# Optimization experiments

Hardware: AMD Instinct MI355X
Metric: run time of the kernel (lower is better)

The kernel has to match this reference:

```python
import jax, jax.numpy as jnp
import numpy as np

D_MODEL = 1024
N_HEAD = 16
B, T = 1, 4096


def setup_inputs() -> dict:
    key = jax.random.key(0)
    ks = jax.random.split(key, 12)
    s = 1.0 / np.sqrt(D_MODEL)
    inp = {
        "q": jax.random.normal(ks[0], (B, T, D_MODEL), jnp.float32),
        "k": jax.random.normal(ks[1], (B, T, D_MODEL), jnp.float32),
        "v": jax.random.normal(ks[2], (B, T, D_MODEL), jnp.float32),
        # causal mask: True = keep, False = mask out (mask==0 path in torch)
        "mask": jnp.tril(jnp.ones((T, T), dtype=bool))[None, None],
        "w_q": jax.random.uniform(ks[3], (D_MODEL, D_MODEL), jnp.float32, -s, s),
        "b_q": jax.random.uniform(ks[4], (D_MODEL,), jnp.float32, -s, s),
        "w_k": jax.random.uniform(ks[5], (D_MODEL, D_MODEL), jnp.float32, -s, s),
        "b_k": jax.random.uniform(ks[6], (D_MODEL,), jnp.float32, -s, s),
        "w_v": jax.random.uniform(ks[7], (D_MODEL, D_MODEL), jnp.float32, -s, s),
        "b_v": jax.random.uniform(ks[8], (D_MODEL,), jnp.float32, -s, s),
        "w_o": jax.random.uniform(ks[9], (D_MODEL, D_MODEL), jnp.float32, -s, s),
        "b_o": jax.random.uniform(ks[10], (D_MODEL,), jnp.float32, -s, s),
    }
    return inp


def reference(q, k, v, mask, w_q, b_q, w_k, b_k, w_v, b_v, w_o, b_o):
    batch, time, d_model = q.shape
    n_d = d_model // N_HEAD
    # Linear projections (torch Linear: x @ W.T + b)
    qh = (q @ w_q.T + b_q).reshape(batch, time, N_HEAD, n_d).transpose(0, 2, 1, 3)
    kh = (k @ w_k.T + b_k).reshape(batch, -1, N_HEAD, n_d).transpose(0, 2, 1, 3)
    vh = (v @ w_v.T + b_v).reshape(batch, -1, N_HEAD, n_d).transpose(0, 2, 1, 3)
    # [B, H, Tq, Tk] score matrix (naive, materialized as in original)
    score = jnp.einsum("bhqd,bhkd->bhqk", qh, kh) / jnp.sqrt(jnp.float32(n_d))
    score = jnp.where(mask, score, jnp.float32(-10000.0))
    attn = jax.nn.softmax(score, axis=-1)
    out = jnp.einsum("bhqk,bhkd->bhqd", attn, vh)
    out = out.transpose(0, 2, 1, 3).reshape(batch, time, d_model)
    return out @ w_o.T + b_o
```

## Files before the change

kernel.cpp:

```cpp
#include <hip/hip_runtime.h>

typedef unsigned short u16;
typedef unsigned int u32;
typedef __bf16 b16x8 __attribute__((ext_vector_type(8)));
typedef float f32x4 __attribute__((ext_vector_type(4)));
typedef u32 u32x4 __attribute__((ext_vector_type(4)));

__device__ __forceinline__ u16 f2b(float f) {
    u32 u = __builtin_bit_cast(u32, f);
    u32 r = (u + 0x7fffu + ((u >> 16) & 1u)) >> 16;
    return (u16)r;
}
__device__ __forceinline__ b16x8 frag(u32x4 x) { return __builtin_bit_cast(b16x8, x); }

__device__ __forceinline__ void gld16(const u16* g, u16* l) {
    __builtin_amdgcn_global_load_lds((const __attribute__((address_space(1))) u32*)g,
                                     (__attribute__((address_space(3))) u32*)l, 16, 0, 0);
}

#define SEQ 4096
#define DMODEL 1024
#define NHEAD 16
#define HDIM 64
#define QK_SCALE 0.18033688011112042f

__global__ void cvt3(const float* __restrict__ s0, const float* __restrict__ s1,
                     const float* __restrict__ s2, u16* __restrict__ d0,
                     u16* __restrict__ d1, u16* __restrict__ d2, int n4) {
    const int t = blockIdx.y;
    const float* s = (t == 0) ? s0 : (t == 1) ? s1 : s2;
    u16* d = (t == 0) ? d0 : (t == 1) ? d1 : d2;
    const int stride = gridDim.x * blockDim.x;
    for (int i = blockIdx.x * blockDim.x + threadIdx.x; i < n4; i += stride) {
        float4 f = ((const float4*)s)[i];
        ushort4 o;
        o.x = f2b(f.x); o.y = f2b(f.y); o.z = f2b(f.z); o.w = f2b(f.w);
        ((ushort4*)d)[i] = o;
    }
}

__global__ void cvt4(const float* __restrict__ s0, const float* __restrict__ s1,
                     const float* __restrict__ s2, const float* __restrict__ s3,
                     u16* __restrict__ d0, u16* __restrict__ d1,
                     u16* __restrict__ d2, u16* __restrict__ d3, int n4) {
    const int t = blockIdx.y;
    const float* s = (t == 0) ? s0 : (t == 1) ? s1 : (t == 2) ? s2 : s3;
    u16* d = (t == 0) ? d0 : (t == 1) ? d1 : (t == 2) ? d2 : d3;
    const int stride = gridDim.x * blockDim.x;
    for (int i = blockIdx.x * blockDim.x + threadIdx.x; i < n4; i += stride) {
        float4 f = ((const float4*)s)[i];
        ushort4 o;
        o.x = f2b(f.x); o.y = f2b(f.y); o.z = f2b(f.z); o.w = f2b(f.w);
        ((ushort4*)d)[i] = o;
    }
}

template <int NN, bool BIAS_ROW, int OUT>
__global__ __launch_bounds__(256) void gemm_bt(const u16* __restrict__ A,
                                               const u16* __restrict__ Bt,
                                               const float* __restrict__ bias,
                                               void* __restrict__ Cv, float scale) {
    constexpr int K = 1024;
    __shared__ __attribute__((aligned(16))) u16 As[128 * 32];
    __shared__ __attribute__((aligned(16))) u16 Bs[128 * 32];

    const int tid = threadIdx.x;
    const int wave = tid >> 6, lane = tid & 63;
    const int quad = lane >> 4, l16 = lane & 15;
    const int wr = wave >> 1, wc = wave & 1;
    const int m0 = blockIdx.y * 128, n0 = blockIdx.x * 128;

    f32x4 acc[4][4] = {};

    const int srow = tid >> 2;
    const int scol = (tid & 3) * 8;
    const u16* Aptr = A + (size_t)(m0 + srow) * K + scol;
    const u16* Bptr = Bt + (size_t)(n0 + srow) * K + scol;
    u16* AsW0 = &As[wave * 512];
    u16* AsW1 = &As[2048 + wave * 512];
    u16* BsW0 = &Bs[wave * 512];
    u16* BsW1 = &Bs[2048 + wave * 512];

    for (int k0 = 0; k0 < K; k0 += 32) {
        __syncthreads();
        gld16(Aptr + k0, AsW0);
        gld16(Aptr + k0 + (size_t)64 * K, AsW1);
        gld16(Bptr + k0, BsW0);
        gld16(Bptr + k0 + (size_t)64 * K, BsW1);
        __syncthreads();

        b16x8 af[4], bf[4];
#pragma unroll
        for (int mt = 0; mt < 4; ++mt)
            af[mt] = frag(*(const u32x4*)&As[(wr * 64 + mt * 16 + l16) * 32 + quad * 8]);
#pragma unroll
        for (int nt = 0; nt < 4; ++nt)
            bf[nt] = frag(*(const u32x4*)&Bs[(wc * 64 + nt * 16 + l16) * 32 + quad * 8]);
#pragma unroll
        for (int mt = 0; mt < 4; ++mt)
#pragma unroll
            for (int nt = 0; nt < 4; ++nt)
                acc[mt][nt] = __builtin_amdgcn_mfma_f32_16x16x32_bf16(af[mt], bf[nt], acc[mt][nt], 0, 0, 0);
    }

#pragma unroll
    for (int nt = 0; nt < 4; ++nt) {
        const int col = n0 + wc * 64 + nt * 16 + l16;
        const float bcol = BIAS_ROW ? 0.f : bias[col];
#pragma unroll
        for (int mt = 0; mt < 4; ++mt) {
            const int row0 = m0 + wr * 64 + mt * 16 + quad * 4;
#pragma unroll
            for (int r = 0; r < 4; ++r) {
                const float bv = BIAS_ROW ? bias[row0 + r] : bcol;
                float v = (acc[mt][nt][r] + bv) * scale;
                if (OUT == 2) {
                    ((float*)Cv)[(size_t)(row0 + r) * NN + col] = v;
                } else if (OUT == 1) {
                    ((u16*)Cv)[((size_t)(col >> 6) * SEQ + (row0 + r)) * HDIM + (col & 63)] = f2b(v);
                } else {
                    ((u16*)Cv)[(size_t)(row0 + r) * NN + col] = f2b(v);
                }
            }
        }
    }
}

__global__ __launch_bounds__(256) void flash_attn(const u16* __restrict__ Q,
                                                  const u16* __restrict__ K,
                                                  const u16* __restrict__ V,
                                                  u16* __restrict__ O) {
    constexpr int LDK = 72;
    __shared__ __attribute__((aligned(16))) u16 Ks[64 * LDK];
    __shared__ __attribute__((aligned(16))) u16 Vs[64 * LDK];
    __shared__ __attribute__((aligned(16))) u16 Ps[128 * LDK];

    const int tid = threadIdx.x;
    const int wave = tid >> 6, lane = tid & 63;
    const int quad = lane >> 4, l16 = lane & 15;

    const int idx = blockIdx.x;
    const int h = idx & (NHEAD - 1);
    const int qt = (SEQ / 128 - 1) - (idx >> 4);
    const int q0 = qt * 128;

    const u16* Qh = Q + (size_t)h * SEQ * HDIM;
    const u16* Kh = K + (size_t)h * SEQ * HDIM;
    const u16* Vh = V + (size_t)h * HDIM * SEQ;

    b16x8 qf[2][2];
#pragma unroll
    for (int mf = 0; mf < 2; ++mf) {
        const u16* qp = Qh + (size_t)(q0 + wave * 32 + mf * 16 + l16) * HDIM + quad * 8;
        qf[mf][0] = frag(*(const u32x4*)qp);
        qf[mf][1] = frag(*(const u32x4*)(qp + 32));
    }
    b16x8 onesf;
    {
        u32x4 o = {0x3F803F80u, 0x3F803F80u, 0x3F803F80u, 0x3F803F80u};
        onesf = frag(o);
    }

    f32x4 acc[2][4] = {};
    f32x4 accl[2] = {};

    const int r0 = tid >> 3;
    const int c0 = (tid & 7) * 8;

    const int nkt = 2 * qt + 2;
    for (int kt = 0; kt < nkt; ++kt) {
        const int k0 = kt * 64;
        u32x4 ka = *(const u32x4*)(Kh + (size_t)(k0 + r0) * HDIM + c0);
        u32x4 kb = *(const u32x4*)(Kh + (size_t)(k0 + r0 + 32) * HDIM + c0);
        u32x4 va = *(const u32x4*)(Vh + (size_t)r0 * SEQ + k0 + c0);
        u32x4 vb = *(const u32x4*)(Vh + (size_t)(r0 + 32) * SEQ + k0 + c0);
        __syncthreads();
        *(u32x4*)&Ks[r0 * LDK + c0] = ka;
        *(u32x4*)&Ks[(r0 + 32) * LDK + c0] = kb;
        *(u32x4*)&Vs[r0 * LDK + c0] = va;
        *(u32x4*)&Vs[(r0 + 32) * LDK + c0] = vb;
        __syncthreads();

        f32x4 s[2][4];
#pragma unroll
        for (int nt = 0; nt < 4; ++nt) {
            b16x8 kf0 = frag(*(const u32x4*)&Ks[(nt * 16 + l16) * LDK + quad * 8]);
            b16x8 kf1 = frag(*(const u32x4*)&Ks[(nt * 16 + l16) * LDK + 32 + quad * 8]);
#pragma unroll
            for (int mf = 0; mf < 2; ++mf) {
                f32x4 z = {};
                z = __builtin_amdgcn_mfma_f32_16x16x32_bf16(qf[mf][0], kf0, z, 0, 0, 0);
                z = __builtin_amdgcn_mfma_f32_16x16x32_bf16(qf[mf][1], kf1, z, 0, 0, 0);
                s[mf][nt] = z;
            }
        }

        if (kt >= 2 * qt) {
#pragma unroll
            for (int nt = 0; nt < 4; ++nt) {
                const int j = k0 + nt * 16 + l16;
#pragma unroll
                for (int mf = 0; mf < 2; ++mf) {
                    const int ib = q0 + wave * 32 + mf * 16 + quad * 4;
#pragma unroll
                    for (int r = 0; r < 4; ++r)
                        if (j > ib + r) s[mf][nt][r] = -1e30f;
                }
            }
        }

#pragma unroll
        for (int mf = 0; mf < 2; ++mf)
#pragma unroll
            for (int nt = 0; nt < 4; ++nt)
#pragma unroll
                for (int r = 0; r < 4; ++r) {
                    const float p = __builtin_amdgcn_exp2f(s[mf][nt][r] - 16.0f);
                    Ps[(wave * 32 + mf * 16 + quad * 4 + r) * LDK + nt * 16 + l16] = f2b(p);
                }
        __syncthreads();

#pragma unroll
        for (int ks = 0; ks < 2; ++ks) {
            b16x8 a[2];
#pragma unroll
            for (int mf = 0; mf < 2; ++mf) {
                a[mf] = frag(*(const u32x4*)&Ps[(wave * 32 + mf * 16 + l16) * LDK + ks * 32 + quad * 8]);
                accl[mf] = __builtin_amdgcn_mfma_f32_16x16x32_bf16(a[mf], onesf, accl[mf], 0, 0, 0);
            }
#pragma unroll
            for (int dt = 0; dt < 4; ++dt) {
                b16x8 b = frag(*(const u32x4*)&Vs[(dt * 16 + l16) * LDK + ks * 32 + quad * 8]);
#pragma unroll
                for (int mf = 0; mf < 2; ++mf)
                    acc[mf][dt] = __builtin_amdgcn_mfma_f32_16x16x32_bf16(a[mf], b, acc[mf][dt], 0, 0, 0);
            }
        }
    }

#pragma unroll
    for (int mf = 0; mf < 2; ++mf)
#pragma unroll
        for (int dt = 0; dt < 4; ++dt)
#pragma unroll
            for (int r = 0; r < 4; ++r) {
                const int row = q0 + wave * 32 + mf * 16 + quad * 4 + r;
                const int col = h * HDIM + dt * 16 + l16;
                O[(size_t)row * DMODEL + col] = f2b(acc[mf][dt][r] / accl[mf][r]);
            }
}

extern "C" void kernel_launch(void* const* d_in, const int* in_sizes, int n_in,
                              void* d_out, int out_size, void* d_ws, size_t ws_size,
                              hipStream_t stream) {
    const float* qkv[3] = {nullptr, nullptr, nullptr};
    const float* wts[4] = {nullptr, nullptr, nullptr, nullptr};
    const float* bss[4] = {nullptr, nullptr, nullptr, nullptr};
    int nqkv = 0, nw = 0, nb = 0;
    for (int i = 0; i < n_in; ++i) {
        const int sz = in_sizes[i];
        if (sz == SEQ * DMODEL) {
            if (nqkv < 3) qkv[nqkv++] = (const float*)d_in[i];
        } else if (sz == DMODEL * DMODEL) {
            if (nw < 4) wts[nw++] = (const float*)d_in[i];
        } else if (sz == DMODEL) {
            if (nb < 4) bss[nb++] = (const float*)d_in[i];
        }
    }

    u16* ws = (u16*)d_ws;
    const size_t ELEMS = (size_t)SEQ * DMODEL;
    const size_t WELEMS = (size_t)DMODEL * DMODEL;

    size_t off = 0;
    u16* cq = ws + off; off += ELEMS;
    u16* ck = ws + off; off += ELEMS;
    u16* cv = ws + off; off += ELEMS;
    u16* cwq = ws + off; off += WELEMS;
    u16* cwk = ws + off; off += WELEMS;
    u16* cwv = ws + off; off += WELEMS;
    u16* cwo = ws + off; off += WELEMS;
    u16* qh = ws + off; off += ELEMS;
    u16* kh = ws + off; off += ELEMS;
    u16* vt = ws + off; off += ELEMS;
    u16* att = ws + off; off += ELEMS;

    dim3 blk(256);
    cvt3<<<dim3(1024, 3), blk, 0, stream>>>(qkv[0], qkv[1], qkv[2], cq, ck, cv,
                                            (int)(ELEMS / 4));
    cvt4<<<dim3(256, 4), blk, 0, stream>>>(wts[0], wts[1], wts[2], wts[3],
                                           cwq, cwk, cwv, cwo, (int)(WELEMS / 4));

    dim3 gM(DMODEL / 128, SEQ / 128);
    dim3 gV(SEQ / 128, DMODEL / 128);
    gemm_bt<DMODEL, false, 1><<<gM, blk, 0, stream>>>(cq, cwq, bss[0], qh, QK_SCALE);
    gemm_bt<DMODEL, false, 1><<<gM, blk, 0, stream>>>(ck, cwk, bss[1], kh, 1.0f);
    gemm_bt<SEQ, true, 0><<<gV, blk, 0, stream>>>(cwv, cv, bss[2], vt, 1.0f);
    flash_attn<<<dim3(NHEAD * (SEQ / 128)), blk, 0, stream>>>(qh, kh, vt, att);
    gemm_bt<DMODEL, false, 2><<<gM, blk, 0, stream>>>(att, cwo, bss[3], d_out, 1.0f);
}
```

Before: 363.1 us.

## Split causal attention KV range across blocks, batch QKV GEMMs, narrow output GEMM

Flash attention now splits the causal key range of the later query tiles into up to four chunks, each handled by its own block. Each block writes unnormalized partial outputs and row sums, and a new combine kernel sums them and normalizes. The aim is to balance the triangular workload and give the GPU more blocks. The three QKV projection GEMMs are merged into one launch over a z dimension, and the output GEMM uses 128x64 tiles so it launches more blocks. The trade-off is an extra kernel plus partial-result traffic through workspace buffers, which reuse the converted input regions.

```diff
diff --git a/kernel.cpp b/kernel.cpp
--- a/kernel.cpp
+++ b/kernel.cpp
@@ -10,6 +10,10 @@
     u32 u = __builtin_bit_cast(u32, f);
     u32 r = (u + 0x7fffu + ((u >> 16) & 1u)) >> 16;
     return (u16)r;
+}
+__device__ __forceinline__ float b2f(u16 h) {
+    u32 u = ((u32)h) << 16;
+    return __builtin_bit_cast(float, u);
 }
 __device__ __forceinline__ b16x8 frag(u32x4 x) { return __builtin_bit_cast(b16x8, x); }
 
@@ -55,20 +59,34 @@
     }
 }
 
-template <int NN, bool BIAS_ROW, int OUT>
-__global__ __launch_bounds__(256) void gemm_bt(const u16* __restrict__ A,
-                                               const u16* __restrict__ Bt,
-                                               const float* __restrict__ bias,
-                                               void* __restrict__ Cv, float scale) {
+__global__ __launch_bounds__(256) void gemm_qkv(
+    const u16* __restrict__ cq, const u16* __restrict__ ck, const u16* __restrict__ cv,
+    const u16* __restrict__ cwq, const u16* __restrict__ cwk, const u16* __restrict__ cwv,
+    const float* __restrict__ bq, const float* __restrict__ bk, const float* __restrict__ bv,
+    u16* __restrict__ qh, u16* __restrict__ kh, u16* __restrict__ vt) {
     constexpr int K = 1024;
     __shared__ __attribute__((aligned(16))) u16 As[128 * 32];
     __shared__ __attribute__((aligned(16))) u16 Bs[128 * 32];
+
+    const int z = blockIdx.z;
+    const u16* A = (z == 0) ? cq : (z == 1) ? ck : cwv;
+    const u16* Bt = (z == 0) ? cwq : (z == 1) ? cwk : cv;
+    const float* bias = (z == 0) ? bq : (z == 1) ? bk : bv;
+
+    int m0, n0;
+    if (z < 2) {
+        m0 = blockIdx.y * 128;
+        n0 = blockIdx.x * 128;
+    } else {
+        const int id = blockIdx.y * 8 + blockIdx.x;
+        m0 = (id >> 5) * 128;
+        n0 = (id & 31) * 128;
+    }
 
     const int tid = threadIdx.x;
     const int wave = tid >> 6, lane = tid & 63;
     const int quad = lane >> 4, l16 = lane & 15;
     const int wr = wave >> 1, wc = wave & 1;
-    const int m0 = blockIdx.y * 128, n0 = blockIdx.x * 128;
 
     f32x4 acc[4][4] = {};
 
@@ -103,25 +121,86 @@
                 acc[mt][nt] = __builtin_amdgcn_mfma_f32_16x16x32_bf16(af[mt], bf[nt], acc[mt][nt], 0, 0, 0);
     }
 
+    u16* C = (z == 0) ? qh : kh;
+    const float sc = (z == 0) ? QK_SCALE : 1.0f;
 #pragma unroll
     for (int nt = 0; nt < 4; ++nt) {
         const int col = n0 + wc * 64 + nt * 16 + l16;
-        const float bcol = BIAS_ROW ? 0.f : bias[col];
+        const float bcol = (z < 2) ? bias[col] : 0.f;
 #pragma unroll
         for (int mt = 0; mt < 4; ++mt) {
             const int row0 = m0 + wr * 64 + mt * 16 + quad * 4;
 #pragma unroll
             for (int r = 0; r < 4; ++r) {
-                const float bv = BIAS_ROW ? bias[row0 + r] : bcol;
-                float v = (acc[mt][nt][r] + bv) * scale;
-                if (OUT == 2) {
-                    ((float*)Cv)[(size_t)(row0 + r) * NN + col] = v;
-                } else if (OUT == 1) {
-                    ((u16*)Cv)[((size_t)(col >> 6) * SEQ + (row0 + r)) * HDIM + (col & 63)] = f2b(v);
+                const int row = row0 + r;
+                float v = acc[mt][nt][r];
+                if (z == 2) {
+                    v += bias[row];
+                    vt[(size_t)row * SEQ + col] = f2b(v);
                 } else {
-                    ((u16*)Cv)[(size_t)(row0 + r) * NN + col] = f2b(v);
+                    v = (v + bcol) * sc;
+                    C[((size_t)(col >> 6) * SEQ + row) * HDIM + (col & 63)] = f2b(v);
                 }
             }
+        }
+    }
+}
+
+__global__ __launch_bounds__(256) void gemm_out(const u16* __restrict__ A,
+                                                const u16* __restrict__ Bt,
+                                                const float* __restrict__ bias,
+                                                float* __restrict__ C) {
+    constexpr int K = 1024, N = 1024;
+    __shared__ __attribute__((aligned(16))) u16 As[128 * 32];
+    __shared__ __attribute__((aligned(16))) u16 Bs[64 * 32];
+
+    const int tid = threadIdx.x;
+    const int wave = tid >> 6, lane = tid & 63;
+    const int quad = lane >> 4, l16 = lane & 15;
+    const int wr = wave >> 1, wc = wave & 1;
+    const int m0 = blockIdx.y * 128, n0 = blockIdx.x * 64;
+
+    f32x4 acc[4][2] = {};
+
+    const int srow = tid >> 2;
+    const int scol = (tid & 3) * 8;
+    const u16* Aptr = A + (size_t)(m0 + srow) * K + scol;
+    const u16* Bptr = Bt + (size_t)(n0 + wave * 16 + (lane >> 2)) * K + (lane & 3) * 8;
+    u16* AsW0 = &As[wave * 512];
+    u16* AsW1 = &As[2048 + wave * 512];
+    u16* BsW = &Bs[wave * 512];
+
+    for (int k0 = 0; k0 < K; k0 += 32) {
+        __syncthreads();
+        gld16(Aptr + k0, AsW0);
+        gld16(Aptr + k0 + (size_t)64 * K, AsW1);
+        gld16(Bptr + k0, BsW);
+        __syncthreads();
+
+        b16x8 af[4], bf[2];
+#pragma unroll
+        for (int mt = 0; mt < 4; ++mt)
+            af[mt] = frag(*(const u32x4*)&As[(wr * 64 + mt * 16 + l16) * 32 + quad * 8]);
+#pragma unroll
+        for (int nt = 0; nt < 2; ++nt)
+            bf[nt] = frag(*(const u32x4*)&Bs[(wc * 32 + nt * 16 + l16) * 32 + quad * 8]);
+#pragma unroll
+        for (int mt = 0; mt < 4; ++mt)
+#pragma unroll
+            for (int nt = 0; nt < 2; ++nt)
+                acc[mt][nt] = __builtin_amdgcn_mfma_f32_16x16x32_bf16(af[mt], bf[nt], acc[mt][nt], 0, 0, 0);
+    }
+
+#pragma unroll
+    for (int nt = 0; nt < 2; ++nt) {
+        const int col = n0 + wc * 32 + nt * 16 + l16;
+        const float bv = bias[col];
+#pragma unroll
+        for (int mt = 0; mt < 4; ++mt) {
+            const int row0 = m0 + wr * 64 + mt * 16 + quad * 4;
+#pragma unroll
+            for (int r = 0; r < 4; ++r)
+                C[(size_t)(row0 + r) * N + col] = acc[mt][nt][r] + bv;
         }
     }
 }
@@ -129,7 +208,8 @@
 __global__ __launch_bounds__(256) void flash_attn(const u16* __restrict__ Q,
                                                   const u16* __restrict__ K,
                                                   const u16* __restrict__ V,
-                                                  u16* __restrict__ O) {
+                                                  u16* __restrict__ pO,
+                                                  float* __restrict__ pL) {
     constexpr int LDK = 72;
     __shared__ __attribute__((aligned(16))) u16 Ks[64 * LDK];
     __shared__ __attribute__((aligned(16))) u16 Vs[64 * LDK];
@@ -139,10 +219,16 @@
     const int wave = tid >> 6, lane = tid & 63;
     const int quad = lane >> 4, l16 = lane & 15;
 
-    const int idx = blockIdx.x;
-    const int h = idx & (NHEAD - 1);
-    const int qt = (SEQ / 128 - 1) - (idx >> 4);
+    const int x = blockIdx.x, h = blockIdx.y;
+    int qt, c, nc;
+    if (x < 8)       { qt = x;                 c = 0;            nc = 1; }
+    else if (x < 24) { qt = 8 + ((x - 8) >> 1);  c = (x - 8) & 1;  nc = 2; }
+    else if (x < 48) { qt = 16 + (x - 24) / 3;   c = (x - 24) % 3; nc = 3; }
+    else             { qt = 24 + ((x - 48) >> 2); c = (x - 48) & 3; nc = 4; }
+    const int nkt = 2 * qt + 2;
+    const int kt0 = (c * nkt) / nc, kt1 = ((c + 1) * nkt) / nc;
     const int q0 = qt * 128;
+    const int slot = h * 80 + x;
 
     const u16* Qh = Q + (size_t)h * SEQ * HDIM;
     const u16* Kh = K + (size_t)h * SEQ * HDIM;
@@ -167,8 +253,7 @@
     const int r0 = tid >> 3;
     const int c0 = (tid & 7) * 8;
 
-    const int nkt = 2 * qt + 2;
-    for (int kt = 0; kt < nkt; ++kt) {
+    for (int kt = kt0; kt < kt1; ++kt) {
         const int k0 = kt * 64;
         u32x4 ka = *(const u32x4*)(Kh + (size_t)(k0 + r0) * HDIM + c0);
         u32x4 kb = *(const u32x4*)(Kh + (size_t)(k0 + r0 + 32) * HDIM + c0);
@@ -238,16 +323,56 @@
         }
     }
 
-#pragma unroll
-    for (int mf = 0; mf < 2; ++mf)
-#pragma unroll
-        for (int dt = 0; dt < 4; ++dt)
-#pragma unroll
-            for (int r = 0; r < 4; ++r) {
-                const int row = q0 + wave * 32 + mf * 16 + quad * 4 + r;
-                const int col = h * HDIM + dt * 16 + l16;
-                O[(size_t)row * DMODEL + col] = f2b(acc[mf][dt][r] / accl[mf][r]);
-            }
+    u16* po = pO + (size_t)slot * 8192;
+#pragma unroll
+    for (int mf = 0; mf < 2; ++mf) {
+        const int row0 = wave * 32 + mf * 16 + quad * 4;
+#pragma unroll
+        for (int dt = 0; dt < 4; ++dt) {
+            const int col = dt * 16 + l16;
+            ushort4 o;
+            o.x = f2b(acc[mf][dt][0]);
+            o.y = f2b(acc[mf][dt][1]);
+            o.z = f2b(acc[mf][dt][2]);
+            o.w = f2b(acc[mf][dt][3]);
+            *(ushort4*)&po[col * 128 + row0] = o;
+        }
+        if (l16 == 0) {
+#pragma unroll
+            for (int r = 0; r < 4; ++r)
+                pL[(size_t)slot * 128 + row0 + r] = accl[mf][r];
+        }
+    }
+}
+
+__global__ __launch_bounds__(256) void combine(const u16* __restrict__ pO,
+                                               const float* __restrict__ pL,
+                                               u16* __restrict__ att) {
+    const int qt = blockIdx.x, h = blockIdx.y;
+    const int g = qt >> 3;
+    const int nc = g + 1;
+    const int slot0 = h * 80 + 4 * g * (g + 1) + (qt - (g << 3)) * nc;
+
+    const int t = threadIdx.x;
+    const int row = t >> 1;
+    const int ch = (t & 1) * 32;
+
+    float lsum = 0.f;
+    for (int cc = 0; cc < nc; ++cc) lsum += pL[(size_t)(slot0 + cc) * 128 + row];
+    const float inv = 1.0f / lsum;
+
+    u16 out[32];
+#pragma unroll 4
+    for (int i = 0; i < 32; ++i) {
+        const int col = ch + i;
+        float o = 0.f;
+        for (int cc = 0; cc < nc; ++cc)
+            o += b2f(pO[(size_t)(slot0 + cc) * 8192 + col * 128 + row]);
+        out[i] = f2b(o * inv);
+    }
+    u16* dst = att + (size_t)(qt * 128 + row) * DMODEL + h * HDIM + ch;
+#pragma unroll
+    for (int i = 0; i < 8; ++i) ((ushort4*)dst)[i] = *(ushort4*)&out[i * 4];
 }
 
 extern "C" void kernel_launch(void* const* d_in, const int* in_sizes, int n_in,
@@ -284,6 +409,8 @@
     u16* kh = ws + off; off += ELEMS;
     u16* vt = ws + off; off += ELEMS;
     u16* att = ws + off; off += ELEMS;
+    u16* pO = cq;
+    float* pL = (float*)cwq;
 
     dim3 blk(256);
     cvt3<<<dim3(1024, 3), blk, 0, stream>>>(qkv[0], qkv[1], qkv[2], cq, ck, cv,
@@ -291,11 +418,9 @@
     cvt4<<<dim3(256, 4), blk, 0, stream>>>(wts[0], wts[1], wts[2], wts[3],
                                            cwq, cwk, cwv, cwo, (int)(WELEMS / 4));
 
-    dim3 gM(DMODEL / 128, SEQ / 128);
-    dim3 gV(SEQ / 128, DMODEL / 128);
-    gemm_bt<DMODEL, false, 1><<<gM, blk, 0, stream>>>(cq, cwq, bss[0], qh, QK_SCALE);
-    gemm_bt<DMODEL, false, 1><<<gM, blk, 0, stream>>>(ck, cwk, bss[1], kh, 1.0f);
-    gemm_bt<SEQ, true, 0><<<gV, blk, 0, stream>>>(cwv, cv, bss[2], vt, 1.0f);
-    flash_attn<<<dim3(NHEAD * (SEQ / 128)), blk, 0, stream>>>(qh, kh, vt, att);
-    gemm_bt<DMODEL, false, 2><<<gM, blk, 0, stream>>>(att, cwo, bss[3], d_out, 1.0f);
-}
+    gemm_qkv<<<dim3(8, 32, 3), blk, 0, stream>>>(cq, ck, cv, cwq, cwk, cwv,
+                                                 bss[0], bss[1], bss[2], qh, kh, vt);
+    flash_attn<<<dim3(80, NHEAD), blk, 0, stream>>>(qh, kh, vt, pO, pL);
+    combine<<<dim3(SEQ / 128, NHEAD), blk, 0, stream>>>(pO, pL, att);
+    gemm_out<<<dim3(16, 32), blk, 0, stream>>>(att, cwo, bss[3], (float*)d_out);
+}
```

After: 368.7 us. Within noise of the previous version (+1.5%).
